# Kernel tuning notes

Hardware: AMD Instinct MI355X
Metric: run time of the kernel (lower is better)

## Reference

```python
import jax, jax.numpy as jnp
import numpy as np

EMBED_DIM = 1024
NUM_HEADS = 16
HEAD_DIM = EMBED_DIM // NUM_HEADS


def setup_inputs() -> dict:
    key = jax.random.key(0)
    ks = jax.random.split(key, 9)
    B, S, E, Hd = 1, 4096, EMBED_DIM, HEAD_DIM
    s = 0.02
    return {
        "x": jax.random.normal(ks[0], (B, S, E), jnp.float32),
        "mask": jnp.ones((B, S, S), jnp.int32),
        "Wq": jax.random.normal(ks[1], (E, E), jnp.float32) * s,
        "bq": jnp.zeros((E,), jnp.float32),
        "Wk": jax.random.normal(ks[2], (E, Hd), jnp.float32) * s,
        "bk": jnp.zeros((Hd,), jnp.float32),
        "Wv": jax.random.normal(ks[3], (E, Hd), jnp.float32) * s,
        "bv": jnp.zeros((Hd,), jnp.float32),
        "Wo": jax.random.normal(ks[4], (E, E), jnp.float32) * s,
        "bo": jnp.zeros((E,), jnp.float32),
    }


def reference(x, mask, Wq, bq, Wk, bk, Wv, bv, Wo, bo):
    B, S, E = x.shape
    H, Hd = NUM_HEADS, HEAD_DIM
    q = (x @ Wq + bq).reshape(B, S, H, Hd).transpose(0, 2, 1, 3)  # [B,H,S,Hd]
    k = x @ Wk + bk  # [B,S,Hd] single KV head (MQA)
    v = x @ Wv + bv  # [B,S,Hd]
    scale = 1.0 / np.sqrt(Hd).astype(np.float32)
    # broadcast single-head K across all query heads
    qk = jnp.einsum('bhqd,bkd->bhqk', q, k) * scale  # [B,H,S,S]
    qk = jnp.where(mask[:, None, :, :] == 0, jnp.float32(-10000.0), qk)
    attn = jax.nn.softmax(qk, axis=-1)
    out = jnp.einsum('bhqk,bkd->bhqd', attn, v)  # [B,H,S,Hd]
    out = out.transpose(0, 2, 1, 3).reshape(B, S, E)
    return out @ Wo + bo
```

## Files before the change

### kernel.cpp

```cpp
#include <hip/hip_runtime.h>
#include <hip/hip_bf16.h>
#include <stdint.h>

typedef __bf16 bf16x8 __attribute__((ext_vector_type(8)));
typedef float f32x4 __attribute__((ext_vector_type(4)));
typedef float f32x16 __attribute__((ext_vector_type(16)));
typedef unsigned int uint2v __attribute__((ext_vector_type(2)));

#define E_DIM 1024
#define HD 64
#define NH 16
#define QKV_LD 1152
#define LOG2E 1.44269504088896f

__device__ __forceinline__ void storeOut(float* p, float v) { *p = v; }
__device__ __forceinline__ void storeOut(__hip_bfloat16* p, float v) { *p = __float2bfloat16(v); }

__device__ __forceinline__ unsigned cvtpk_bf16(float lo, float hi_) {
    unsigned r;
    asm("v_cvt_pk_bf16_f32 %0, %1, %2" : "=v"(r) : "v"(lo), "v"(hi_));
    return r;
}
__device__ __forceinline__ void perm32swap(unsigned& a, unsigned& b) {
    uint2v r = __builtin_amdgcn_permlane32_swap(a, b, false, false);
    a = r.x; b = r.y;
}
__device__ __forceinline__ float fexp2(float x) {
    float r;
    asm("v_exp_f32 %0, %1" : "=v"(r) : "v"(x));
    return r;
}

typedef __attribute__((address_space(1))) void gvoid;
typedef __attribute__((address_space(3))) void lvoid;
__device__ __forceinline__ void gload_lds16(const void* g, void* l) {
    __builtin_amdgcn_global_load_lds((gvoid*)g, (lvoid*)l, 16, 0, 0);
}

__global__ __launch_bounds__(256)
void prep_kernel(const float* __restrict__ x, __hip_bfloat16* __restrict__ xb,
                 const int* __restrict__ mask, unsigned long long* __restrict__ mbits,
                 const float* __restrict__ Wq, const float* __restrict__ Wk,
                 const float* __restrict__ Wv, const float* __restrict__ Wo,
                 __hip_bfloat16* __restrict__ wqkvT, __hip_bfloat16* __restrict__ woT,
                 const float* __restrict__ bq, const float* __restrict__ bk,
                 const float* __restrict__ bv, float* __restrict__ bqkv,
                 int S) {
    __shared__ float tile[32][33];
    const int tid = threadIdx.x;
    const int castBlocks = S * E_DIM / 1024;
    const int maskBlocks = 1024;
    int bid = blockIdx.x;

    if (bid < castBlocks) {
        int i = (bid * 256 + tid) * 4;
        float4 v = *reinterpret_cast<const float4*>(x + i);
        __hip_bfloat16 t[4] = {__float2bfloat16(v.x), __float2bfloat16(v.y),
                               __float2bfloat16(v.z), __float2bfloat16(v.w)};
        *reinterpret_cast<uint2*>(xb + i) = *reinterpret_cast<uint2*>(t);
        return;
    }
    bid -= castBlocks;
    if (bid < maskBlocks) {
        int gtid = bid * 256 + tid;
        int wid = gtid >> 6, lane = gtid & 63;
        int nw = (maskBlocks * 256) >> 6;
        int nwords = S * (S / 64);
        for (int w = wid; w < nwords; w += nw) {
            int v = mask[(size_t)w * 64 + lane];
            unsigned long long b = __ballot(v != 0);
            if (lane == 0) mbits[w] = b;
        }
        return;
    }
    bid -= maskBlocks;
    if (bid < 2176) {
        const float* in; __hip_bfloat16* out; int ldi, bx, by;
        if (bid < 1024)      { in = Wq; out = wqkvT;                                ldi = E_DIM; bx = bid >> 5; by = bid & 31; }
        else if (bid < 1088) { int t2 = bid - 1024;
                               in = Wk; out = wqkvT + (size_t)E_DIM * E_DIM;        ldi = HD;    bx = t2 >> 1;  by = t2 & 1; }
        else if (bid < 1152) { int t2 = bid - 1088;
                               in = Wv; out = wqkvT + (size_t)(E_DIM + HD) * E_DIM; ldi = HD;    bx = t2 >> 1;  by = t2 & 1; }
        else                 { int t2 = bid - 1152;
                               in = Wo; out = woT;                                  ldi = E_DIM; bx = t2 >> 5; by = t2 & 31; }
        const int tx = tid & 31, ty = tid >> 5;
#pragma unroll
        for (int j = 0; j < 4; ++j) {
            int r = bx * 32 + ty + j * 8, c = by * 32 + tx;
            tile[ty + j * 8][tx] = in[(size_t)r * ldi + c];
        }
        __syncthreads();
#pragma unroll
        for (int j = 0; j < 4; ++j) {
            int c = by * 32 + ty + j * 8, r = bx * 32 + tx;
            out[(size_t)c * E_DIM + r] = __float2bfloat16(tile[tx][ty + j * 8]);
        }
        return;
    }
    for (int i = tid; i < E_DIM + 2 * HD; i += 256)
        bqkv[i] = (i < E_DIM) ? bq[i] : (i < E_DIM + HD ? bk[i - E_DIM] : bv[i - E_DIM - HD]);
}

template<typename OutT, bool VTB>
__global__ __launch_bounds__(256)
void gemm_bt3_kernel(const __hip_bfloat16* __restrict__ A,
                     const __hip_bfloat16* __restrict__ Bt,
                     const float* __restrict__ bias,
                     OutT* __restrict__ C,
                     __hip_bfloat16* __restrict__ vtb,
                     int M, int N, int K, float sQ, int nQ, float sKV) {
    constexpr int BM = 64, BN = 128, BK = 64;
    __shared__ __align__(16) unsigned char lA[2][BM * BK * 2];
    __shared__ __align__(16) unsigned char lB[2][BN * BK * 2];
    const int ntn = N / BN;
    const int tm = blockIdx.x / ntn, tn = blockIdx.x % ntn;
    const int tid = threadIdx.x, lane = tid & 63, wave = tid >> 6;
    const int l15 = lane & 15, l4 = lane >> 4;
    const int wm = (wave >> 1) * 32, wn = (wave & 1) * 64;
    const int r0 = tm * BM, c0 = tn * BN;
    const int NK = K / BK;

    size_t aoff[2]; unsigned ldsoA[2];
    size_t boff[4]; unsigned ldsoB[4];
#pragma unroll
    for (int i = 0; i < 2; ++i) {
        int row = wave * 16 + i * 8 + (lane >> 3);
        int c = (lane & 7) ^ (row & 7);
        aoff[i] = (size_t)(r0 + row) * K * 2 + c * 16;
        ldsoA[i] = wave * 2048 + i * 1024;
    }
#pragma unroll
    for (int i = 0; i < 4; ++i) {
        int row = wave * 32 + i * 8 + (lane >> 3);
        int c = (lane & 7) ^ (row & 7);
        boff[i] = (size_t)(c0 + row) * K * 2 + c * 16;
        ldsoB[i] = wave * 4096 + i * 1024;
    }
    const char* Ab = (const char*)A;
    const char* Bb = (const char*)Bt;

#pragma unroll
    for (int i = 0; i < 2; ++i) gload_lds16(Ab + aoff[i], &lA[0][ldsoA[i]]);
#pragma unroll
    for (int i = 0; i < 4; ++i) gload_lds16(Bb + boff[i], &lB[0][ldsoB[i]]);
    __syncthreads();

    f32x4 z4 = {0.f, 0.f, 0.f, 0.f};
    f32x4 acc[2][4];
#pragma unroll
    for (int mi = 0; mi < 2; ++mi)
#pragma unroll
        for (int ni = 0; ni < 4; ++ni) acc[mi][ni] = z4;

    int buf = 0;
    for (int ks = 0; ks < NK; ++ks) {
        if (ks + 1 < NK) {
            size_t kb = (size_t)(ks + 1) * BK * 2;
#pragma unroll
            for (int i = 0; i < 2; ++i) gload_lds16(Ab + aoff[i] + kb, &lA[buf ^ 1][ldsoA[i]]);
#pragma unroll
            for (int i = 0; i < 4; ++i) gload_lds16(Bb + boff[i] + kb, &lB[buf ^ 1][ldsoB[i]]);
        }
        bf16x8 af[2][2], bf[4][2];
#pragma unroll
        for (int mi = 0; mi < 2; ++mi) {
            int row = wm + mi * 16 + l15;
#pragma unroll
            for (int kh = 0; kh < 2; ++kh) {
                int slot = (kh * 4 + l4) ^ (row & 7);
                af[mi][kh] = *reinterpret_cast<const bf16x8*>(&lA[buf][row * 128 + slot * 16]);
            }
        }
#pragma unroll
        for (int ni = 0; ni < 4; ++ni) {
            int row = wn + ni * 16 + l15;
#pragma unroll
            for (int kh = 0; kh < 2; ++kh) {
                int slot = (kh * 4 + l4) ^ (row & 7);
                bf[ni][kh] = *reinterpret_cast<const bf16x8*>(&lB[buf][row * 128 + slot * 16]);
            }
        }
        __builtin_amdgcn_s_setprio(1);
#pragma unroll
        for (int mi = 0; mi < 2; ++mi)
#pragma unroll
            for (int ni = 0; ni < 4; ++ni) {
                acc[mi][ni] = __builtin_amdgcn_mfma_f32_16x16x32_bf16(af[mi][0], bf[ni][0], acc[mi][ni], 0, 0, 0);
                acc[mi][ni] = __builtin_amdgcn_mfma_f32_16x16x32_bf16(af[mi][1], bf[ni][1], acc[mi][ni], 0, 0, 0);
            }
        __builtin_amdgcn_s_setprio(0);
        __syncthreads();
        buf ^= 1;
    }

#pragma unroll
    for (int ni = 0; ni < 4; ++ni) {
        int col = c0 + wn + ni * 16 + l15;
        float b = bias[col];
        float s = (col < nQ) ? sQ : sKV;
#pragma unroll
        for (int mi = 0; mi < 2; ++mi) {
            int row = r0 + wm + mi * 16 + l4 * 4;
#pragma unroll
            for (int r = 0; r < 4; ++r) {
                float v = (acc[mi][ni][r] + b) * s;
                storeOut(C + (size_t)(row + r) * N + col, v);
                if constexpr (VTB) {
                    if (col >= nQ + HD)
                        vtb[(size_t)(col - nQ - HD) * M + row + r] = __float2bfloat16(v);
                }
            }
        }
    }
}

__global__ __launch_bounds__(256, 2)
void mqa10_kernel(const __hip_bfloat16* __restrict__ qkv,
                  const __hip_bfloat16* __restrict__ vtb,
                  const unsigned long long* __restrict__ mbits,
                  __hip_bfloat16* __restrict__ attnb,
                  int S) {
    __shared__ __align__(16) unsigned char sKV[2][32768];
    const int tid = threadIdx.x, lane = tid & 63, w = tid >> 6;
    const int r31 = lane & 31, hi = lane >> 5, rx = r31 & 15;
    const int q0 = blockIdx.x * 32;
    const int h = blockIdx.y * 4 + w;
    const int NT = S / 128, NW64 = S / 64;
    const __hip_bfloat16* kvb = qkv + E_DIM;

    bf16x8 qf[4];
    {
        const __hip_bfloat16* qp = qkv + (size_t)(q0 + r31) * QKV_LD + h * HD + hi * 8;
#pragma unroll
        for (int s = 0; s < 4; ++s) qf[s] = *reinterpret_cast<const bf16x8*>(qp + 16 * s);
    }
    bf16x8 ones;
#pragma unroll
    for (int i = 0; i < 8; ++i) ones[i] = (__bf16)1.0f;

    const char* gbase[8];
    int gstep[8];
    unsigned ldsoff[8];
#pragma unroll
    for (int i = 0; i < 8; ++i) {
        int r = w * 32 + i * 4 + (lane >> 4);
        int sl = lane & 15;
        int c = sl ^ (r & 15);
        if (c < 8) {
            gbase[i] = (const char*)(kvb + (size_t)r * QKV_LD + c * 8);
            gstep[i] = 128 * QKV_LD * 2;
        } else {
            gbase[i] = (const char*)(vtb + (size_t)(r & 63) * S + (r >> 6) * 64 + (c - 8) * 8);
            gstep[i] = 128 * 2;
        }
        ldsoff[i] = w * 8192 + i * 1024;
    }

#pragma unroll
    for (int i = 0; i < 8; ++i) { gload_lds16(gbase[i], &sKV[0][ldsoff[i]]); gbase[i] += gstep[i]; }
    __syncthreads();

    f32x16 oacc[2], lacc;
#pragma unroll
    for (int i = 0; i < 16; ++i) { oacc[0][i] = 0.f; oacc[1][i] = 0.f; lacc[i] = 0.f; }

    const size_t mrow = (size_t)(q0 + r31) * NW64;
    int buf = 0;
    for (int t = 0; t < NT; ++t) {
        ulonglong2 wb = *reinterpret_cast<const ulonglong2*>(mbits + mrow + 2 * t);
        if (t + 1 < NT) {
#pragma unroll
            for (int i = 0; i < 8; ++i) { gload_lds16(gbase[i], &sKV[buf ^ 1][ldsoff[i]]); gbase[i] += gstep[i]; }
        }
        const unsigned char* bp = sKV[buf];

        f32x16 sacc[4];
        __builtin_amdgcn_s_setprio(1);
#pragma unroll
        for (int kb = 0; kb < 4; ++kb) {
            const unsigned char* rowp = bp + (kb * 32 + r31) * 256;
            f32x16 a;
#pragma unroll
            for (int i = 0; i < 16; ++i) a[i] = 0.f;
#pragma unroll
            for (int s = 0; s < 4; ++s) {
                int slot = (2 * s + hi) ^ rx;
                bf16x8 kf = *reinterpret_cast<const bf16x8*>(rowp + slot * 16);
                a = __builtin_amdgcn_mfma_f32_32x32x16_bf16(kf, qf[s], a, 0, 0, 0);
            }
            sacc[kb] = a;
        }
        __builtin_amdgcn_s_setprio(0);

        if ((wb.x & wb.y) != ~0ull) {
#pragma unroll
            for (int kb = 0; kb < 4; ++kb) {
                unsigned long long wv = (kb < 2) ? wb.x : wb.y;
                int base = (kb & 1) * 32;
#pragma unroll
                for (int r = 0; r < 16; ++r) {
                    int kl = base + (r & 3) + 8 * (r >> 2) + 4 * hi;
                    if (!((wv >> kl) & 1)) sacc[kb][r] = -14427.0f;
                }
            }
        }

#pragma unroll
        for (int kb = 0; kb < 4; ++kb)
#pragma unroll
            for (int r = 0; r < 16; ++r) sacc[kb][r] = fexp2(sacc[kb][r]);

#pragma unroll
        for (int j = 0; j < 2; ++j) {
            bf16x8 pa[4];
#pragma unroll
            for (int kk = 0; kk < 2; ++kk) {
#pragma unroll
                for (int half = 0; half < 2; ++half) {
                    int b0 = half * 8;
                    const f32x16& sv = sacc[2 * j + kk];
                    unsigned A = cvtpk_bf16(sv[b0 + 0], sv[b0 + 1]);
                    unsigned B = cvtpk_bf16(sv[b0 + 2], sv[b0 + 3]);
                    unsigned C = cvtpk_bf16(sv[b0 + 4], sv[b0 + 5]);
                    unsigned D = cvtpk_bf16(sv[b0 + 6], sv[b0 + 7]);
                    perm32swap(A, C);
                    perm32swap(B, D);
                    union { unsigned u[4]; bf16x8 v; } pk;
                    pk.u[0] = A; pk.u[1] = B; pk.u[2] = C; pk.u[3] = D;
                    pa[kk * 2 + half] = pk.v;
                }
            }
            __builtin_amdgcn_s_setprio(1);
#pragma unroll
            for (int db = 0; db < 2; ++db) {
                const unsigned char* rowp = bp + (j * 64 + db * 32 + r31) * 256;
                f32x16 a = oacc[db];
#pragma unroll
                for (int s = 0; s < 4; ++s) {
                    int slot = (8 + 2 * s + hi) ^ rx;
                    bf16x8 vf = *reinterpret_cast<const bf16x8*>(rowp + slot * 16);
                    a = __builtin_amdgcn_mfma_f32_32x32x16_bf16(vf, pa[s], a, 0, 0, 0);
                }
                oacc[db] = a;
            }
#pragma unroll
            for (int s = 0; s < 4; ++s)
                lacc = __builtin_amdgcn_mfma_f32_32x32x16_bf16(ones, pa[s], lacc, 0, 0, 0);
            __builtin_amdgcn_s_setprio(0);
        }

        __syncthreads();
        buf ^= 1;
    }

    float inv = 1.0f / lacc[0];
    __hip_bfloat16* op = attnb + (size_t)(q0 + r31) * E_DIM + h * HD;
#pragma unroll
    for (int db = 0; db < 2; ++db)
#pragma unroll
        for (int m = 0; m < 4; ++m) {
            uint2 pk;
            pk.x = cvtpk_bf16(oacc[db][4 * m + 0] * inv, oacc[db][4 * m + 1] * inv);
            pk.y = cvtpk_bf16(oacc[db][4 * m + 2] * inv, oacc[db][4 * m + 3] * inv);
            *reinterpret_cast<uint2*>(op + db * 32 + m * 8 + hi * 4) = pk;
        }
}

extern "C" void kernel_launch(void* const* d_in, const int* in_sizes, int n_in,
                              void* d_out, int out_size, void* d_ws, size_t ws_size,
                              hipStream_t stream) {
    (void)n_in; (void)out_size; (void)ws_size;
    const float* x  = (const float*)d_in[0];
    const int* mask = (const int*)d_in[1];
    const float* Wq = (const float*)d_in[2];
    const float* bq = (const float*)d_in[3];
    const float* Wk = (const float*)d_in[4];
    const float* bk = (const float*)d_in[5];
    const float* Wv = (const float*)d_in[6];
    const float* bv = (const float*)d_in[7];
    const float* Wo = (const float*)d_in[8];
    const float* bo = (const float*)d_in[9];
    float* out = (float*)d_out;

    const int E = E_DIM;
    const int S = in_sizes[0] / E;

    char* ws = (char*)d_ws;
    size_t off = 0;
    auto alloc = [&](size_t b) { char* p = ws + off; off += (b + 255) & ~(size_t)255; return p; };
    __hip_bfloat16* xb     = (__hip_bfloat16*)alloc((size_t)S * E * 2);
    __hip_bfloat16* wqkvT  = (__hip_bfloat16*)alloc((size_t)QKV_LD * E * 2);
    __hip_bfloat16* woT    = (__hip_bfloat16*)alloc((size_t)E * E * 2);
    __hip_bfloat16* qkvb   = (__hip_bfloat16*)alloc((size_t)S * QKV_LD * 2);
    __hip_bfloat16* vtb    = (__hip_bfloat16*)alloc((size_t)HD * S * 2);
    __hip_bfloat16* attnb  = (__hip_bfloat16*)alloc((size_t)S * E * 2);
    float* bqkv  = (float*)alloc(QKV_LD * 4);
    unsigned long long* mbits = (unsigned long long*)alloc((size_t)S * (S / 64) * 8);

    const int prepBlocks = (S * E / 1024) + 1024 + 2176 + 1;
    prep_kernel<<<dim3(prepBlocks), dim3(256), 0, stream>>>(
        x, xb, mask, mbits, Wq, Wk, Wv, Wo, wqkvT, woT, bq, bk, bv, bqkv, S);

    gemm_bt3_kernel<__hip_bfloat16, true><<<dim3((S / 64) * (QKV_LD / 128)), dim3(256), 0, stream>>>(
        xb, wqkvT, bqkv, qkvb, vtb, S, QKV_LD, E, 0.125f * LOG2E, E, 1.0f);
    mqa10_kernel<<<dim3(S / 32, NH / 4), dim3(256), 0, stream>>>(qkvb, vtb, mbits, attnb, S);
    gemm_bt3_kernel<float, false><<<dim3((S / 64) * (E / 128)), dim3(256), 0, stream>>>(
        attnb, woT, bo, out, nullptr, S, E, E, 1.0f, E, 1.0f);
}
```

Measured before the change: 158.6 us.

## Split KV sequence across two wave groups per block with LDS reduction

The attention kernel now launches 512 threads per block. Two groups of four waves each process alternating 128-key tiles, so both LDS buffers are consumed at the same time instead of being double-buffered. The loads for the next pair of tiles are issued after a barrier, and the partial outputs and row sums are combined through LDS at the end. This doubles the waves working on each query tile to raise latency hiding and occupancy. In exchange, the overlap between global loads and compute is lost, and a second barrier per iteration plus a final reduction are added.

```diff
diff --git a/kernel.cpp b/kernel.cpp
--- a/kernel.cpp
+++ b/kernel.cpp
@@ -214,18 +214,20 @@
     }
 }
 
-__global__ __launch_bounds__(256, 2)
-void mqa10_kernel(const __hip_bfloat16* __restrict__ qkv,
+__global__ __launch_bounds__(512, 4)
+void mqa12_kernel(const __hip_bfloat16* __restrict__ qkv,
                   const __hip_bfloat16* __restrict__ vtb,
                   const unsigned long long* __restrict__ mbits,
                   __hip_bfloat16* __restrict__ attnb,
                   int S) {
     __shared__ __align__(16) unsigned char sKV[2][32768];
     const int tid = threadIdx.x, lane = tid & 63, w = tid >> 6;
+    const int hw = w & 3, parity = w >> 2;
     const int r31 = lane & 31, hi = lane >> 5, rx = r31 & 15;
     const int q0 = blockIdx.x * 32;
-    const int h = blockIdx.y * 4 + w;
-    const int NT = S / 128, NW64 = S / 64;
+    const int h = blockIdx.y * 4 + hw;
+    const int NW64 = S / 64;
+    const int NP = S / 256;
     const __hip_bfloat16* kvb = qkv + E_DIM;
 
     bf16x8 qf[4];
@@ -243,17 +245,18 @@
     unsigned ldsoff[8];
 #pragma unroll
     for (int i = 0; i < 8; ++i) {
-        int r = w * 32 + i * 4 + (lane >> 4);
+        int b = i >> 2;
+        int r = w * 16 + (i & 3) * 4 + (lane >> 4);
         int sl = lane & 15;
         int c = sl ^ (r & 15);
         if (c < 8) {
-            gbase[i] = (const char*)(kvb + (size_t)r * QKV_LD + c * 8);
-            gstep[i] = 128 * QKV_LD * 2;
+            gbase[i] = (const char*)(kvb + (size_t)(b * 128 + r) * QKV_LD + c * 8);
+            gstep[i] = 256 * QKV_LD * 2;
         } else {
-            gbase[i] = (const char*)(vtb + (size_t)(r & 63) * S + (r >> 6) * 64 + (c - 8) * 8);
-            gstep[i] = 128 * 2;
-        }
-        ldsoff[i] = w * 8192 + i * 1024;
+            gbase[i] = (const char*)(vtb + (size_t)(r & 63) * S + b * 128 + (r >> 6) * 64 + (c - 8) * 8);
+            gstep[i] = 256 * 2;
+        }
+        ldsoff[i] = b * 32768 + w * 4096 + (i & 3) * 1024;
     }
 
 #pragma unroll
@@ -265,14 +268,10 @@
     for (int i = 0; i < 16; ++i) { oacc[0][i] = 0.f; oacc[1][i] = 0.f; lacc[i] = 0.f; }
 
     const size_t mrow = (size_t)(q0 + r31) * NW64;
-    int buf = 0;
-    for (int t = 0; t < NT; ++t) {
+    const unsigned char* bp = &sKV[parity][0];
+    for (int it = 0; it < NP; ++it) {
+        const int t = 2 * it + parity;
         ulonglong2 wb = *reinterpret_cast<const ulonglong2*>(mbits + mrow + 2 * t);
-        if (t + 1 < NT) {
-#pragma unroll
-            for (int i = 0; i < 8; ++i) { gload_lds16(gbase[i], &sKV[buf ^ 1][ldsoff[i]]); gbase[i] += gstep[i]; }
-        }
-        const unsigned char* bp = sKV[buf];
 
         f32x16 sacc[4];
         __builtin_amdgcn_s_setprio(1);
@@ -350,20 +349,36 @@
         }
 
         __syncthreads();
-        buf ^= 1;
-    }
-
-    float inv = 1.0f / lacc[0];
-    __hip_bfloat16* op = attnb + (size_t)(q0 + r31) * E_DIM + h * HD;
-#pragma unroll
-    for (int db = 0; db < 2; ++db)
-#pragma unroll
-        for (int m = 0; m < 4; ++m) {
-            uint2 pk;
-            pk.x = cvtpk_bf16(oacc[db][4 * m + 0] * inv, oacc[db][4 * m + 1] * inv);
-            pk.y = cvtpk_bf16(oacc[db][4 * m + 2] * inv, oacc[db][4 * m + 3] * inv);
-            *reinterpret_cast<uint2*>(op + db * 32 + m * 8 + hi * 4) = pk;
-        }
+        if (it + 1 < NP) {
+#pragma unroll
+            for (int i = 0; i < 8; ++i) { gload_lds16(gbase[i], &sKV[0][ldsoff[i]]); gbase[i] += gstep[i]; }
+        }
+        __syncthreads();
+    }
+
+    float* eps = (float*)&sKV[0][0];
+    float* slot = eps + ((size_t)(hw * 64 + lane) * 34);
+    if (parity == 1) {
+#pragma unroll
+        for (int i = 0; i < 16; ++i) { slot[i] = oacc[0][i]; slot[16 + i] = oacc[1][i]; }
+        slot[32] = lacc[0];
+    }
+    __syncthreads();
+    if (parity == 0) {
+#pragma unroll
+        for (int i = 0; i < 16; ++i) { oacc[0][i] += slot[i]; oacc[1][i] += slot[16 + i]; }
+        float inv = 1.0f / (lacc[0] + slot[32]);
+        __hip_bfloat16* op = attnb + (size_t)(q0 + r31) * E_DIM + h * HD;
+#pragma unroll
+        for (int db = 0; db < 2; ++db)
+#pragma unroll
+            for (int m = 0; m < 4; ++m) {
+                uint2 pk;
+                pk.x = cvtpk_bf16(oacc[db][4 * m + 0] * inv, oacc[db][4 * m + 1] * inv);
+                pk.y = cvtpk_bf16(oacc[db][4 * m + 2] * inv, oacc[db][4 * m + 3] * inv);
+                *reinterpret_cast<uint2*>(op + db * 32 + m * 8 + hi * 4) = pk;
+            }
+    }
 }
 
 extern "C" void kernel_launch(void* const* d_in, const int* in_sizes, int n_in,
@@ -403,7 +418,7 @@
 
     gemm_bt3_kernel<__hip_bfloat16, true><<<dim3((S / 64) * (QKV_LD / 128)), dim3(256), 0, stream>>>(
         xb, wqkvT, bqkv, qkvb, vtb, S, QKV_LD, E, 0.125f * LOG2E, E, 1.0f);
-    mqa10_kernel<<<dim3(S / 32, NH / 4), dim3(256), 0, stream>>>(qkvb, vtb, mbits, attnb, S);
+    mqa12_kernel<<<dim3(S / 32, NH / 4), dim3(512), 0, stream>>>(qkvb, vtb, mbits, attnb, S);
     gemm_bt3_kernel<float, false><<<dim3((S / 64) * (E / 128)), dim3(256), 0, stream>>>(
         attnb, woT, bo, out, nullptr, S, E, E, 1.0f, E, 1.0f);
 }
```

Result: slower. 552.7 us (+248.4%).
